# Performance work log

Hardware: AMD Instinct MI355X
Metric: run time of the kernel (lower is better)

The kernel has to match this reference:

```python
import jax, jax.numpy as jnp
import numpy as np

N = 4096
D_IN = 1024
D_OUT = 1024
NUM_HEADS = 16
HEAD_DIM = D_OUT // NUM_HEADS


def setup_inputs() -> dict:
    key = jax.random.key(0)
    ks = jax.random.split(key, 7)
    scale = 1.0 / np.sqrt(D_IN)
    return {
        "q": jax.random.normal(ks[0], (N, D_IN), dtype=jnp.float32),
        "k": jax.random.normal(ks[1], (N, D_IN), dtype=jnp.float32),
        "v": jax.random.normal(ks[2], (N, D_IN), dtype=jnp.float32),
        "W_q": jax.random.normal(ks[3], (D_IN, D_OUT), dtype=jnp.float32) * scale,
        "W_k": jax.random.normal(ks[4], (D_IN, D_OUT), dtype=jnp.float32) * scale,
        "W_v": jax.random.normal(ks[5], (D_IN, D_OUT), dtype=jnp.float32) * scale,
        "W_o": jax.random.normal(ks[6], (D_OUT, D_OUT), dtype=jnp.float32) * scale,
    }


def reference(q, k, v, W_q, W_k, W_v, W_o):
    n = q.shape[0]
    # QKV projections -> [h, n, d]
    Q = (q @ W_q).reshape(n, NUM_HEADS, HEAD_DIM).transpose(1, 0, 2)
    K = (k @ W_k).reshape(n, NUM_HEADS, HEAD_DIM).transpose(1, 0, 2)
    V = (v @ W_v).reshape(n, NUM_HEADS, HEAD_DIM).transpose(1, 0, 2)
    scores = jnp.einsum('hid,hjd->hij', Q, K) / jnp.sqrt(jnp.float32(HEAD_DIM))
    attn = jax.nn.softmax(scores, axis=-1)  # dropout p=0.0 (eval) -> no-op
    h = jnp.einsum('hij,hjd->hid', attn, V)
    h = h.transpose(1, 0, 2).reshape(n, D_OUT)
    return h @ W_o
```

## Files before the change

kernel.cpp:

```cpp
#include <hip/hip_runtime.h>
#include <math.h>

#define NTOK   4096
#define DMODEL 1024
#define NHEADS 16
#define HDIM   64
#define KDIM   1024

typedef __attribute__((ext_vector_type(8))) short          bf16x8;
typedef __attribute__((ext_vector_type(4))) float          f32x4;
typedef __attribute__((ext_vector_type(16))) float         f32x16;
typedef __attribute__((ext_vector_type(4))) unsigned int   u32x4;
typedef __attribute__((ext_vector_type(4))) unsigned short us4;

static __device__ __forceinline__ unsigned short f2bf(float f) {
    unsigned int u = __float_as_uint(f);
    u += 0x7fffu + ((u >> 16) & 1u);
    return (unsigned short)(u >> 16);
}

static __device__ __forceinline__ unsigned int pk2bf(float a, float b) {
#if __has_builtin(__builtin_amdgcn_cvt_pk_bf16_f32)
    return __builtin_bit_cast(unsigned int,
                              __builtin_amdgcn_cvt_pk_bf16_f32(a, b));
#else
    unsigned int ua = __float_as_uint(a) + 0x8000u;
    unsigned int ub = __float_as_uint(b) + 0x8000u;
    return __builtin_amdgcn_perm(ub, ua, 0x07060302u);
#endif
}

#if __has_builtin(__builtin_amdgcn_exp2f)
#define EXP2(x) __builtin_amdgcn_exp2f(x)
#else
#define EXP2(x) exp2f(x)
#endif

static __device__ __forceinline__ void async_copy16(void* lds, const void* g) {
    __builtin_amdgcn_global_load_lds(
        (const __attribute__((address_space(1))) unsigned int*)g,
        (__attribute__((address_space(3))) unsigned int*)lds, 16, 0, 0);
}

static __device__ __forceinline__ unsigned int comb2(unsigned int x,
                                                     unsigned int y,
                                                     float inv) {
    float x0 = __uint_as_float(x << 16);
    float x1 = __uint_as_float(x & 0xffff0000u);
    float y0 = __uint_as_float(y << 16);
    float y1 = __uint_as_float(y & 0xffff0000u);
    return pk2bf((x0 + y0) * inv, (x1 + y1) * inv);
}

__global__ __launch_bounds__(256)
void cast_wt_kernel(const float* __restrict__ Wq, const float* __restrict__ Wk,
                    const float* __restrict__ Wv, const float* __restrict__ Wo,
                    unsigned short* __restrict__ Tq, unsigned short* __restrict__ Tk,
                    unsigned short* __restrict__ Tv, unsigned short* __restrict__ To) {
    __shared__ float Ws[64][65];
    const float* W;
    unsigned short* T;
    switch (blockIdx.z) {
        case 0:  W = Wq; T = Tq; break;
        case 1:  W = Wk; T = Tk; break;
        case 2:  W = Wv; T = Tv; break;
        default: W = Wo; T = To; break;
    }
    const int k0 = blockIdx.x * 64, n0 = blockIdx.y * 64;
    const int t = threadIdx.x;
    #pragma unroll
    for (int i = 0; i < 4; i++) {
        int c  = i * 256 + t;
        int kk = c >> 4;
        int n4 = (c & 15) << 2;
        *(float4*)(&Ws[kk][n4]) =
            *(const float4*)(W + (size_t)(k0 + kk) * DMODEL + n0 + n4);
    }
    __syncthreads();
    #pragma unroll
    for (int i = 0; i < 4; i++) {
        int c  = i * 256 + t;
        int nn = c >> 4;
        int k4 = (c & 15) << 2;
        us4 o = { f2bf(Ws[k4 + 0][nn]), f2bf(Ws[k4 + 1][nn]),
                  f2bf(Ws[k4 + 2][nn]), f2bf(Ws[k4 + 3][nn]) };
        *(us4*)(T + (size_t)(n0 + nn) * KDIM + k0 + k4) = o;
    }
}

__global__ __launch_bounds__(256)
void cast_in_kernel(const float* __restrict__ q, const float* __restrict__ k,
                    const float* __restrict__ v,
                    unsigned short* __restrict__ Qb,
                    unsigned short* __restrict__ Kb,
                    unsigned short* __restrict__ Vb) {
    const float* src;
    unsigned short* dst;
    switch (blockIdx.y) {
        case 0:  src = q; dst = Qb; break;
        case 1:  src = k; dst = Kb; break;
        default: src = v; dst = Vb; break;
    }
    size_t i = ((size_t)blockIdx.x * 256 + threadIdx.x) * 8;
    float4 f0 = *(const float4*)(src + i);
    float4 f1 = *(const float4*)(src + i + 4);
    uint2 o0 = { pk2bf(f0.x, f0.y), pk2bf(f0.z, f0.w) };
    uint2 o1 = { pk2bf(f1.x, f1.y), pk2bf(f1.z, f1.w) };
    *(uint2*)(dst + i)     = o0;
    *(uint2*)(dst + i + 4) = o1;
}

__global__ __launch_bounds__(256, 3)
void qkv_gemm_pre(const unsigned short* __restrict__ Qb,
                  const unsigned short* __restrict__ Kb,
                  const unsigned short* __restrict__ Vb,
                  const unsigned short* __restrict__ Btq,
                  const unsigned short* __restrict__ Btk,
                  const unsigned short* __restrict__ Btv,
                  unsigned short* __restrict__ Oq, unsigned short* __restrict__ Ok,
                  unsigned short* __restrict__ Ov) {
    __shared__ unsigned short As[128 * 64];
    __shared__ unsigned short Bs[128 * 64];

    const unsigned short* A;
    const unsigned short* Bt;
    unsigned short* Out;
    int mode;
    float sc;
    switch (blockIdx.z) {
        case 0:  A = Qb; Bt = Btq; Out = Oq; mode = 1; sc = 0.18033688011112042f; break;
        case 1:  A = Kb; Bt = Btk; Out = Ok; mode = 1; sc = 1.0f; break;
        default: A = Vb; Bt = Btv; Out = Ov; mode = 2; sc = 1.0f; break;
    }

    const int t    = threadIdx.x;
    const int w    = t >> 6;
    const int lane = t & 63;
    const int quad = lane >> 4;
    const int l15  = lane & 15;
    const int wr   = w >> 1, wc = w & 1;
    const int bm   = blockIdx.y * 128, bn = blockIdx.x * 128;

    f32x4 acc[4][4];
    #pragma unroll
    for (int i = 0; i < 4; i++)
        #pragma unroll
        for (int j = 0; j < 4; j++) acc[i][j] = (f32x4)(0.f);

    for (int k0 = 0; k0 < KDIM; k0 += 64) {
        __syncthreads();
        #pragma unroll
        for (int i = 0; i < 4; i++) {
            int cb = (i * 4 + w) * 64;
            int c  = cb + lane;
            int r  = c >> 3;
            int ko = (c & 7) * 8;
            async_copy16((void*)(Bs + cb * 8),
                         (const void*)(Bt + (size_t)(bn + r) * KDIM + k0 + ko));
            async_copy16((void*)(As + cb * 8),
                         (const void*)(A + (size_t)(bm + r) * KDIM + k0 + ko));
        }
        __syncthreads();
        #pragma unroll
        for (int kq = 0; kq < 2; kq++) {
            bf16x8 af[4], bf[4];
            #pragma unroll
            for (int mt = 0; mt < 4; mt++)
                af[mt] = *(bf16x8*)(As + (wr * 64 + mt * 16 + l15) * 64 + kq * 32 + quad * 8);
            #pragma unroll
            for (int nt = 0; nt < 4; nt++)
                bf[nt] = *(bf16x8*)(Bs + (wc * 64 + nt * 16 + l15) * 64 + kq * 32 + quad * 8);
            #pragma unroll
            for (int mt = 0; mt < 4; mt++)
                #pragma unroll
                for (int nt = 0; nt < 4; nt++)
                    acc[mt][nt] = __builtin_amdgcn_mfma_f32_16x16x32_bf16(
                        af[mt], bf[nt], acc[mt][nt], 0, 0, 0);
        }
    }

    #pragma unroll
    for (int mt = 0; mt < 4; mt++) {
        #pragma unroll
        for (int nt = 0; nt < 4; nt++) {
            int col  = bn + wc * 64 + nt * 16 + l15;
            int row0 = bm + wr * 64 + mt * 16 + quad * 4;
            if (mode == 1) {
                size_t base = ((size_t)(col >> 6)) * NTOK * HDIM + (col & 63);
                #pragma unroll
                for (int r = 0; r < 4; r++)
                    Out[base + (size_t)(row0 + r) * HDIM] = f2bf(acc[mt][nt][r] * sc);
            } else {
                size_t base = ((size_t)(col >> 6)) * HDIM * NTOK +
                              (size_t)(col & 63) * NTOK + row0;
                us4 o = { f2bf(acc[mt][nt][0]), f2bf(acc[mt][nt][1]),
                          f2bf(acc[mt][nt][2]), f2bf(acc[mt][nt][3]) };
                *(us4*)(Out + base) = o;
            }
        }
    }
}

__global__ __launch_bounds__(256, 3)
void qkv_gemm(const float* __restrict__ Aq, const float* __restrict__ Ak,
              const float* __restrict__ Av,
              const unsigned short* __restrict__ Btq,
              const unsigned short* __restrict__ Btk,
              const unsigned short* __restrict__ Btv,
              unsigned short* __restrict__ Oq, unsigned short* __restrict__ Ok,
              unsigned short* __restrict__ Ov) {
    __shared__ unsigned short As[128 * 64];
    __shared__ unsigned short Bs[128 * 64];

    const float* A;
    const unsigned short* Bt;
    unsigned short* Out;
    int mode;
    float sc;
    switch (blockIdx.z) {
        case 0:  A = Aq; Bt = Btq; Out = Oq; mode = 1; sc = 0.18033688011112042f; break;
        case 1:  A = Ak; Bt = Btk; Out = Ok; mode = 1; sc = 1.0f; break;
        default: A = Av; Bt = Btv; Out = Ov; mode = 2; sc = 1.0f; break;
    }

    const int t    = threadIdx.x;
    const int w    = t >> 6;
    const int lane = t & 63;
    const int quad = lane >> 4;
    const int l15  = lane & 15;
    const int wr   = w >> 1, wc = w & 1;
    const int bm   = blockIdx.y * 128, bn = blockIdx.x * 128;

    f32x4 acc[4][4];
    #pragma unroll
    for (int i = 0; i < 4; i++)
        #pragma unroll
        for (int j = 0; j < 4; j++) acc[i][j] = (f32x4)(0.f);

    for (int k0 = 0; k0 < KDIM; k0 += 64) {
        __syncthreads();
        #pragma unroll
        for (int i = 0; i < 4; i++) {
            int cb = (i * 4 + w) * 64;
            int c  = cb + lane;
            int r  = c >> 3;
            int ko = (c & 7) * 8;
            async_copy16((void*)(Bs + cb * 8),
                         (const void*)(Bt + (size_t)(bn + r) * KDIM + k0 + ko));
        }
        #pragma unroll
        for (int i = 0; i < 4; i++) {
            int c2 = i * 256 + t;
            int r  = c2 >> 3;
            int k8 = (c2 & 7) * 8;
            const float* src = A + (size_t)(bm + r) * KDIM + k0 + k8;
            float4 f0 = *(const float4*)(src);
            float4 f1 = *(const float4*)(src + 4);
            uint2 p0 = { pk2bf(f0.x, f0.y), pk2bf(f0.z, f0.w) };
            uint2 p1 = { pk2bf(f1.x, f1.y), pk2bf(f1.z, f1.w) };
            *(uint2*)(As + r * 64 + k8)     = p0;
            *(uint2*)(As + r * 64 + k8 + 4) = p1;
        }
        __syncthreads();
        #pragma unroll
        for (int kq = 0; kq < 2; kq++) {
            bf16x8 af[4], bf[4];
            #pragma unroll
            for (int mt = 0; mt < 4; mt++)
                af[mt] = *(bf16x8*)(As + (wr * 64 + mt * 16 + l15) * 64 + kq * 32 + quad * 8);
            #pragma unroll
            for (int nt = 0; nt < 4; nt++)
                bf[nt] = *(bf16x8*)(Bs + (wc * 64 + nt * 16 + l15) * 64 + kq * 32 + quad * 8);
            #pragma unroll
            for (int mt = 0; mt < 4; mt++)
                #pragma unroll
                for (int nt = 0; nt < 4; nt++)
                    acc[mt][nt] = __builtin_amdgcn_mfma_f32_16x16x32_bf16(
                        af[mt], bf[nt], acc[mt][nt], 0, 0, 0);
        }
    }

    #pragma unroll
    for (int mt = 0; mt < 4; mt++) {
        #pragma unroll
        for (int nt = 0; nt < 4; nt++) {
            int col  = bn + wc * 64 + nt * 16 + l15;
            int row0 = bm + wr * 64 + mt * 16 + quad * 4;
            if (mode == 1) {
                size_t base = ((size_t)(col >> 6)) * NTOK * HDIM + (col & 63);
                #pragma unroll
                for (int r = 0; r < 4; r++)
                    Out[base + (size_t)(row0 + r) * HDIM] = f2bf(acc[mt][nt][r] * sc);
            } else {
                size_t base = ((size_t)(col >> 6)) * HDIM * NTOK +
                              (size_t)(col & 63) * NTOK + row0;
                us4 o = { f2bf(acc[mt][nt][0]), f2bf(acc[mt][nt][1]),
                          f2bf(acc[mt][nt][2]), f2bf(acc[mt][nt][3]) };
                *(us4*)(Out + base) = o;
            }
        }
    }
}

__global__ __launch_bounds__(256, 3)
void out_gemm(const unsigned short* __restrict__ A,
              const unsigned short* __restrict__ Bt,
              float* __restrict__ Out) {
    __shared__ unsigned short As[64 * 64];
    __shared__ unsigned short Bs[128 * 64];

    const int t    = threadIdx.x;
    const int w    = t >> 6;
    const int lane = t & 63;
    const int quad = lane >> 4;
    const int l15  = lane & 15;
    const int wr   = w >> 1, wc = w & 1;
    const int bm   = blockIdx.y * 64, bn = blockIdx.x * 128;

    f32x4 acc[2][4];
    #pragma unroll
    for (int i = 0; i < 2; i++)
        #pragma unroll
        for (int j = 0; j < 4; j++) acc[i][j] = (f32x4)(0.f);

    for (int k0 = 0; k0 < KDIM; k0 += 64) {
        __syncthreads();
        #pragma unroll
        for (int i = 0; i < 4; i++) {
            int cb = (i * 4 + w) * 64;
            int c  = cb + lane;
            int r  = c >> 3;
            int ko = (c & 7) * 8;
            async_copy16((void*)(Bs + cb * 8),
                         (const void*)(Bt + (size_t)(bn + r) * KDIM + k0 + ko));
        }
        #pragma unroll
        for (int i = 0; i < 2; i++) {
            int cb = (i * 4 + w) * 64;
            int c  = cb + lane;
            int r  = c >> 3;
            int ko = (c & 7) * 8;
            async_copy16((void*)(As + cb * 8),
                         (const void*)(A + (size_t)(bm + r) * KDIM + k0 + ko));
        }
        __syncthreads();
        #pragma unroll
        for (int kq = 0; kq < 2; kq++) {
            bf16x8 af[2], bf[4];
            #pragma unroll
            for (int mt = 0; mt < 2; mt++)
                af[mt] = *(bf16x8*)(As + (wr * 32 + mt * 16 + l15) * 64 + kq * 32 + quad * 8);
            #pragma unroll
            for (int nt = 0; nt < 4; nt++)
                bf[nt] = *(bf16x8*)(Bs + (wc * 64 + nt * 16 + l15) * 64 + kq * 32 + quad * 8);
            #pragma unroll
            for (int mt = 0; mt < 2; mt++)
                #pragma unroll
                for (int nt = 0; nt < 4; nt++)
                    acc[mt][nt] = __builtin_amdgcn_mfma_f32_16x16x32_bf16(
                        af[mt], bf[nt], acc[mt][nt], 0, 0, 0);
        }
    }

    #pragma unroll
    for (int mt = 0; mt < 2; mt++) {
        #pragma unroll
        for (int nt = 0; nt < 4; nt++) {
            int col  = bn + wc * 64 + nt * 16 + l15;
            int row0 = bm + wr * 32 + mt * 16 + quad * 4;
            #pragma unroll
            for (int r = 0; r < 4; r++)
                Out[(size_t)(row0 + r) * DMODEL + col] = acc[mt][nt][r];
        }
    }
}

__global__ __launch_bounds__(256, 3)
void out_gemm_comb(const unsigned short* __restrict__ POa,
                   const float* __restrict__ lbuf,
                   const unsigned short* __restrict__ Bt,
                   float* __restrict__ Out) {
    __shared__ unsigned short As[64 * 64];
    __shared__ unsigned short Bs[128 * 64];

    const unsigned short* POb = POa + (size_t)NTOK * DMODEL;

    const int t    = threadIdx.x;
    const int w    = t >> 6;
    const int lane = t & 63;
    const int quad = lane >> 4;
    const int l15  = lane & 15;
    const int wr   = w >> 1, wc = w & 1;
    const int bm   = blockIdx.y * 64, bn = blockIdx.x * 128;

    f32x4 acc[2][4];
    #pragma unroll
    for (int i = 0; i < 2; i++)
        #pragma unroll
        for (int j = 0; j < 4; j++) acc[i][j] = (f32x4)(0.f);

    for (int k0 = 0; k0 < KDIM; k0 += 64) {
        __syncthreads();
        #pragma unroll
        for (int i = 0; i < 4; i++) {
            int cb = (i * 4 + w) * 64;
            int c  = cb + lane;
            int r  = c >> 3;
            int ko = (c & 7) * 8;
            async_copy16((void*)(Bs + cb * 8),
                         (const void*)(Bt + (size_t)(bn + r) * KDIM + k0 + ko));
        }
        #pragma unroll
        for (int i = 0; i < 2; i++) {
            int c   = i * 256 + t;
            int r   = c >> 3;
            int k8  = (c & 7) * 8;
            size_t row = (size_t)(bm + r);
            int col = k0 + k8;
            int hh  = col >> 6;
            uint4 a = *(const uint4*)(POa + row * DMODEL + col);
            uint4 b = *(const uint4*)(POb + row * DMODEL + col);
            float la = lbuf[(size_t)hh * NTOK + row];
            float lb = lbuf[(size_t)NHEADS * NTOK + (size_t)hh * NTOK + row];
            float inv = 1.f / (la + lb);
            uint4 o = { comb2(a.x, b.x, inv), comb2(a.y, b.y, inv),
                        comb2(a.z, b.z, inv), comb2(a.w, b.w, inv) };
            *(uint4*)(As + r * 64 + k8) = o;
        }
        __syncthreads();
        #pragma unroll
        for (int kq = 0; kq < 2; kq++) {
            bf16x8 af[2], bf[4];
            #pragma unroll
            for (int mt = 0; mt < 2; mt++)
                af[mt] = *(bf16x8*)(As + (wr * 32 + mt * 16 + l15) * 64 + kq * 32 + quad * 8);
            #pragma unroll
            for (int nt = 0; nt < 4; nt++)
                bf[nt] = *(bf16x8*)(Bs + (wc * 64 + nt * 16 + l15) * 64 + kq * 32 + quad * 8);
            #pragma unroll
            for (int mt = 0; mt < 2; mt++)
                #pragma unroll
                for (int nt = 0; nt < 4; nt++)
                    acc[mt][nt] = __builtin_amdgcn_mfma_f32_16x16x32_bf16(
                        af[mt], bf[nt], acc[mt][nt], 0, 0, 0);
        }
    }

    #pragma unroll
    for (int mt = 0; mt < 2; mt++) {
        #pragma unroll
        for (int nt = 0; nt < 4; nt++) {
            int col  = bn + wc * 64 + nt * 16 + l15;
            int row0 = bm + wr * 32 + mt * 16 + quad * 4;
            #pragma unroll
            for (int r = 0; r < 4; r++)
                Out[(size_t)(row0 + r) * DMODEL + col] = acc[mt][nt][r];
        }
    }
}

__global__ __launch_bounds__(256, 4)
void attn_split(const unsigned short* __restrict__ Q,
                const unsigned short* __restrict__ K,
                const unsigned short* __restrict__ Vt,
                unsigned short* __restrict__ PO,
                float* __restrict__ lbuf) {
    __shared__ __align__(16) unsigned short Ks[2 * 4096];
    __shared__ __align__(16) unsigned short Vs[2 * 4096];

    const int qt   = blockIdx.x;
    const int h    = blockIdx.y;
    const int half = blockIdx.z;
    const int t    = threadIdx.x;
    const int w    = t >> 6;
    const int lane = t & 63;
    const int r    = lane & 31;
    const int hi   = lane >> 5;
    const int xh   = (r & 7) ^ hi;

    const unsigned short* Qg =
        Q + ((size_t)h * NTOK + qt * 128 + w * 32 + r) * HDIM + hi * 8;
    bf16x8 qf[4];
    #pragma unroll
    for (int ds = 0; ds < 4; ds++)
        qf[ds] = *(const bf16x8*)(Qg + ds * 16);

    const unsigned short* Kg = K  + ((size_t)h * NTOK + half * 2048) * HDIM;
    const unsigned short* Vg = Vt + (size_t)h * HDIM * NTOK + half * 2048;

    const int rr = t >> 3;
    const int oo = ((t & 7) ^ (rr & 7)) * 8;
    const unsigned short* kbase = Kg + (size_t)rr * HDIM + oo;
    const unsigned short* vbase = Vg + (size_t)rr * NTOK + oo;
    unsigned short* ksd = Ks + w * 512;
    unsigned short* vsd = Vs + w * 512;

    auto stage = [&](int kt, int b) {
        const unsigned short* kp = kbase + (size_t)kt * 64 * HDIM;
        const unsigned short* vp = vbase + kt * 64;
        async_copy16((void*)(ksd + b * 4096),        (const void*)kp);
        async_copy16((void*)(ksd + b * 4096 + 2048), (const void*)(kp + 32 * HDIM));
        async_copy16((void*)(vsd + b * 4096),        (const void*)vp);
        async_copy16((void*)(vsd + b * 4096 + 2048), (const void*)(vp + (size_t)32 * NTOK));
    };

    f32x16 O0 = (f32x16)(0.f), O1 = (f32x16)(0.f);
    float l0 = 0.f, l1 = 0.f, l2 = 0.f, l3 = 0.f;

    stage(0, 0);

    for (int kt = 0; kt < 32; kt++) {
        const int cur = kt & 1;
        __syncthreads();
        if (kt + 1 < 32) stage(kt + 1, cur ^ 1);

        const unsigned short* Kb = Ks + cur * 4096 + r * 64;
        const unsigned short* Vb = Vs + cur * 4096 + r * 64;

        f32x16 S0 = (f32x16)(0.f), S1 = (f32x16)(0.f);
        #pragma unroll
        for (int ds = 0; ds < 4; ds++) {
            int c = ((2 * ds) ^ xh) * 8;
            bf16x8 k0 = *(const bf16x8*)(Kb + c);
            bf16x8 k1 = *(const bf16x8*)(Kb + 2048 + c);
            S0 = __builtin_amdgcn_mfma_f32_32x32x16_bf16(k0, qf[ds], S0, 0, 0, 0);
            S1 = __builtin_amdgcn_mfma_f32_32x32x16_bf16(k1, qf[ds], S1, 0, 0, 0);
        }

        #pragma unroll
        for (int kb = 0; kb < 2; kb++) {
            const f32x16 S = kb ? S1 : S0;
            float p[16];
            #pragma unroll
            for (int i = 0; i < 16; i++) p[i] = EXP2(S[i]);
            #pragma unroll
            for (int i = 0; i < 4; i++) {
                l0 += p[i * 4 + 0];
                l1 += p[i * 4 + 1];
                l2 += p[i * 4 + 2];
                l3 += p[i * 4 + 3];
            }
            #pragma unroll
            for (int g = 0; g < 2; g++) {
                unsigned int w0 = pk2bf(p[g * 8 + 0], p[g * 8 + 1]);
                unsigned int w2 = pk2bf(p[g * 8 + 4], p[g * 8 + 5]);
                unsigned int w1 = pk2bf(p[g * 8 + 2], p[g * 8 + 3]);
                unsigned int w3 = pk2bf(p[g * 8 + 6], p[g * 8 + 7]);
                asm volatile("v_permlane32_swap_b32 %0, %1" : "+v"(w0), "+v"(w2));
                asm volatile("v_permlane32_swap_b32 %0, %1" : "+v"(w1), "+v"(w3));
                u32x4 pw = { w0, w1, w2, w3 };
                bf16x8 pf = __builtin_bit_cast(bf16x8, pw);
                int kg = kb * 2 + g;
                int c  = ((2 * kg) ^ xh) * 8;
                bf16x8 v0 = *(const bf16x8*)(Vb + c);
                bf16x8 v1 = *(const bf16x8*)(Vb + 2048 + c);
                O0 = __builtin_amdgcn_mfma_f32_32x32x16_bf16(v0, pf, O0, 0, 0, 0);
                O1 = __builtin_amdgcn_mfma_f32_32x32x16_bf16(v1, pf, O1, 0, 0, 0);
            }
        }
    }

    float lt  = (l0 + l1) + (l2 + l3);
    float ltot = lt + __shfl_xor(lt, 32, 64);

    unsigned short* POh = PO + (size_t)half * NTOK * DMODEL;
    size_t row = (size_t)qt * 128 + w * 32 + r;
    unsigned short* dst = POh + row * DMODEL + h * HDIM;
    #pragma unroll
    for (int db = 0; db < 2; db++) {
        const f32x16 O = db ? O1 : O0;
        #pragma unroll
        for (int g = 0; g < 4; g++) {
            int d = db * 32 + g * 8 + hi * 4;
            uint2 o = { pk2bf(O[g * 4 + 0], O[g * 4 + 1]),
                        pk2bf(O[g * 4 + 2], O[g * 4 + 3]) };
            *(uint2*)(dst + d) = o;
        }
    }
    if (hi == 0)
        lbuf[((size_t)half * NHEADS + h) * NTOK + row] = ltot;
}

__global__ __launch_bounds__(256)
void attn_mfma(const unsigned short* __restrict__ Q,
               const unsigned short* __restrict__ K,
               const unsigned short* __restrict__ Vt,
               unsigned short* __restrict__ ctx) {
    __shared__ __align__(16) unsigned short Ks[2 * 4096];
    __shared__ __align__(16) unsigned short Vs[2 * 4096];
    __shared__ __align__(16) unsigned short Ps[4][32][72];

    const int h    = blockIdx.y;
    const int qt   = blockIdx.x;
    const int t    = threadIdx.x;
    const int w    = t >> 6;
    const int lane = t & 63;
    const int quad = lane >> 4;
    const int l15  = lane & 15;

    const unsigned short* Qg =
        Q + ((size_t)h * NTOK + qt * 128 + w * 32 + l15) * HDIM;
    bf16x8 qf[2][2];
    qf[0][0] = *(const bf16x8*)(Qg + quad * 8);
    qf[0][1] = *(const bf16x8*)(Qg + 32 + quad * 8);
    qf[1][0] = *(const bf16x8*)(Qg + 16 * HDIM + quad * 8);
    qf[1][1] = *(const bf16x8*)(Qg + 16 * HDIM + 32 + quad * 8);

    const unsigned short* Kg = K  + (size_t)h * NTOK * HDIM;
    const unsigned short* Vg = Vt + (size_t)h * HDIM * NTOK;

    const int rr = t >> 3;
    const int oo = ((t & 7) ^ (rr & 7)) * 8;
    const unsigned short* kbase = Kg + (size_t)rr * HDIM + oo;
    const unsigned short* vbase = Vg + (size_t)rr * NTOK + oo;
    unsigned short* ksd = Ks + w * 512;
    unsigned short* vsd = Vs + w * 512;

    auto stage = [&](int kt, int b) {
        const unsigned short* kp = kbase + (size_t)kt * 64 * HDIM;
        const unsigned short* vp = vbase + kt * 64;
        async_copy16((void*)(ksd + b * 4096),        (const void*)kp);
        async_copy16((void*)(ksd + b * 4096 + 2048), (const void*)(kp + 32 * HDIM));
        async_copy16((void*)(vsd + b * 4096),        (const void*)vp);
        async_copy16((void*)(vsd + b * 4096 + 2048), (const void*)(vp + (size_t)32 * NTOK));
    };

    const int xb = l15 & 7;
    const int a0 = l15 * 64 + ((quad    ) ^ xb) * 8;
    const int a1 = l15 * 64 + ((quad + 4) ^ xb) * 8;

    const bf16x8 ones = { 16256, 16256, 16256, 16256,
                          16256, 16256, 16256, 16256 };

    f32x4 O[2][4];
    f32x4 lacc[2];
    #pragma unroll
    for (int tl = 0; tl < 2; tl++) {
        lacc[tl] = (f32x4)(0.f);
        #pragma unroll
        for (int dt = 0; dt < 4; dt++) O[tl][dt] = (f32x4)(0.f);
    }

    stage(0, 0);

    for (int kt = 0; kt < NTOK / 64; kt++) {
        const int cur = kt & 1;
        __syncthreads();
        if (kt + 1 < NTOK / 64) stage(kt + 1, cur ^ 1);

        f32x4 s[2][4];
        #pragma unroll
        for (int kc = 0; kc < 4; kc++) {
            bf16x8 kf0 = *(bf16x8*)(Ks + cur * 4096 + kc * 1024 + a0);
            bf16x8 kf1 = *(bf16x8*)(Ks + cur * 4096 + kc * 1024 + a1);
            #pragma unroll
            for (int tl = 0; tl < 2; tl++) {
                f32x4 acc = (f32x4)(0.f);
                acc = __builtin_amdgcn_mfma_f32_16x16x32_bf16(kf0, qf[tl][0], acc, 0, 0, 0);
                acc = __builtin_amdgcn_mfma_f32_16x16x32_bf16(kf1, qf[tl][1], acc, 0, 0, 0);
                s[tl][kc] = acc;
            }
        }

        bf16x8 vf[4][2];
        #pragma unroll
        for (int dt = 0; dt < 4; dt++) {
            vf[dt][0] = *(bf16x8*)(Vs + cur * 4096 + dt * 1024 + a0);
            vf[dt][1] = *(bf16x8*)(Vs + cur * 4096 + dt * 1024 + a1);
        }

        #pragma unroll
        for (int tl = 0; tl < 2; tl++) {
            #pragma unroll
            for (int kc = 0; kc < 4; kc++) {
                float e0 = EXP2(s[tl][kc][0]);
                float e1 = EXP2(s[tl][kc][1]);
                float e2 = EXP2(s[tl][kc][2]);
                float e3 = EXP2(s[tl][kc][3]);
                uint2 p = { pk2bf(e0, e1), pk2bf(e2, e3) };
                *(uint2*)(&Ps[w][tl * 16 + l15][kc * 16 + quad * 4]) = p;
            }
            asm volatile("s_waitcnt lgkmcnt(0)" ::: "memory");

            bf16x8 pf0 = *(bf16x8*)(&Ps[w][tl * 16 + l15][quad * 8]);
            bf16x8 pf1 = *(bf16x8*)(&Ps[w][tl * 16 + l15][32 + quad * 8]);
            lacc[tl] = __builtin_amdgcn_mfma_f32_16x16x32_bf16(ones, pf0, lacc[tl], 0, 0, 0);
            lacc[tl] = __builtin_amdgcn_mfma_f32_16x16x32_bf16(ones, pf1, lacc[tl], 0, 0, 0);
            #pragma unroll
            for (int dt = 0; dt < 4; dt++) {
                O[tl][dt] = __builtin_amdgcn_mfma_f32_16x16x32_bf16(vf[dt][0], pf0, O[tl][dt], 0, 0, 0);
                O[tl][dt] = __builtin_amdgcn_mfma_f32_16x16x32_bf16(vf[dt][1], pf1, O[tl][dt], 0, 0, 0);
            }
        }
    }

    #pragma unroll
    for (int tl = 0; tl < 2; tl++) {
        float inv = 1.f / lacc[tl][0];
        size_t row = (size_t)qt * 128 + w * 32 + tl * 16 + l15;
        #pragma unroll
        for (int dt = 0; dt < 4; dt++) {
            uint2 o = { pk2bf(O[tl][dt][0] * inv, O[tl][dt][1] * inv),
                        pk2bf(O[tl][dt][2] * inv, O[tl][dt][3] * inv) };
            *(uint2*)(ctx + row * DMODEL + h * HDIM + dt * 16 + quad * 4) = o;
        }
    }
}

extern "C" void kernel_launch(void* const* d_in, const int* in_sizes, int n_in,
                              void* d_out, int out_size, void* d_ws, size_t ws_size,
                              hipStream_t stream) {
    const float* q  = (const float*)d_in[0];
    const float* k  = (const float*)d_in[1];
    const float* v  = (const float*)d_in[2];
    const float* Wq = (const float*)d_in[3];
    const float* Wk = (const float*)d_in[4];
    const float* Wv = (const float*)d_in[5];
    const float* Wo = (const float*)d_in[6];
    float* out = (float*)d_out;

    unsigned short* WqT = (unsigned short*)d_ws;
    unsigned short* WkT = WqT + (size_t)DMODEL * KDIM;
    unsigned short* WvT = WkT + (size_t)DMODEL * KDIM;
    unsigned short* WoT = WvT + (size_t)DMODEL * KDIM;
    unsigned short* Qh  = WoT + (size_t)DMODEL * KDIM;
    unsigned short* Kh  = Qh  + (size_t)NTOK * DMODEL;
    unsigned short* Vth = Kh  + (size_t)NTOK * DMODEL;
    unsigned short* ctx = Vth + (size_t)NTOK * DMODEL;
    unsigned short* Qb  = ctx + (size_t)NTOK * DMODEL;
    unsigned short* Kb  = Qb  + (size_t)NTOK * DMODEL;
    unsigned short* Vb  = Kb  + (size_t)NTOK * DMODEL;
    unsigned short* PO  = Qb;
    float*          lb  = (float*)(PO + (size_t)2 * NTOK * DMODEL);

    const bool bigws = ws_size >= (size_t)67108864;

    cast_wt_kernel<<<dim3(16, 16, 4), 256, 0, stream>>>(Wq, Wk, Wv, Wo,
                                                        WqT, WkT, WvT, WoT);
    if (bigws) {
        cast_in_kernel<<<dim3(2048, 3), 256, 0, stream>>>(q, k, v, Qb, Kb, Vb);
        qkv_gemm_pre<<<dim3(DMODEL / 128, NTOK / 128, 3), 256, 0, stream>>>(
            Qb, Kb, Vb, WqT, WkT, WvT, Qh, Kh, Vth);
        attn_split<<<dim3(NTOK / 128, NHEADS, 2), 256, 0, stream>>>(
            Qh, Kh, Vth, PO, lb);
        out_gemm_comb<<<dim3(DMODEL / 128, NTOK / 64), 256, 0, stream>>>(
            PO, lb, WoT, out);
    } else {
        qkv_gemm<<<dim3(DMODEL / 128, NTOK / 128, 3), 256, 0, stream>>>(
            q, k, v, WqT, WkT, WvT, Qh, Kh, Vth);
        attn_mfma<<<dim3(NTOK / 128, NHEADS), 256, 0, stream>>>(Qh, Kh, Vth, ctx);
        out_gemm<<<dim3(DMODEL / 128, NTOK / 64), 256, 0, stream>>>(ctx, WoT, out);
    }
}
```

Baseline: 257.8 us.

## Halve attn_split block and KV tile to 64 queries and 32 keys

The split-KV attention kernel now runs 128-thread blocks covering 64 query rows, and streams 32-key K/V tiles over 64 iterations instead of 64-key tiles over 32. The staging swizzle and shared-memory layout are reworked for the narrower V tile. The grid doubles, so more blocks are resident per CU and each uses less LDS, which should help occupancy and latency hiding. In exchange, each loaded K/V tile is shared by fewer query rows, so global/L2 traffic per query rises, and there are twice as many barriers per block.

```diff
diff --git a/kernel.cpp b/kernel.cpp
--- a/kernel.cpp
+++ b/kernel.cpp
@@ -459,14 +459,14 @@
     }
 }
 
-__global__ __launch_bounds__(256, 4)
+__global__ __launch_bounds__(128, 4)
 void attn_split(const unsigned short* __restrict__ Q,
                 const unsigned short* __restrict__ K,
                 const unsigned short* __restrict__ Vt,
                 unsigned short* __restrict__ PO,
                 float* __restrict__ lbuf) {
-    __shared__ __align__(16) unsigned short Ks[2 * 4096];
-    __shared__ __align__(16) unsigned short Vs[2 * 4096];
+    __shared__ __align__(16) unsigned short Ks[2 * 2048];
+    __shared__ __align__(16) unsigned short Vs[2 * 2048];
 
     const int qt   = blockIdx.x;
     const int h    = blockIdx.y;
@@ -476,10 +476,11 @@
     const int lane = t & 63;
     const int r    = lane & 31;
     const int hi   = lane >> 5;
-    const int xh   = (r & 7) ^ hi;
+    const int xh8  = (r & 7) ^ hi;
+    const int xh4  = (r & 3) ^ hi;
 
     const unsigned short* Qg =
-        Q + ((size_t)h * NTOK + qt * 128 + w * 32 + r) * HDIM + hi * 8;
+        Q + ((size_t)h * NTOK + qt * 64 + w * 32 + r) * HDIM + hi * 8;
     bf16x8 qf[4];
     #pragma unroll
     for (int ds = 0; ds < 4; ds++)
@@ -488,20 +489,23 @@
     const unsigned short* Kg = K  + ((size_t)h * NTOK + half * 2048) * HDIM;
     const unsigned short* Vg = Vt + (size_t)h * HDIM * NTOK + half * 2048;
 
-    const int rr = t >> 3;
-    const int oo = ((t & 7) ^ (rr & 7)) * 8;
-    const unsigned short* kbase = Kg + (size_t)rr * HDIM + oo;
-    const unsigned short* vbase = Vg + (size_t)rr * NTOK + oo;
+    const int krow = t >> 3;
+    const int koo  = ((t & 7) ^ (krow & 7)) * 8;
+    const unsigned short* kbase = Kg + (size_t)krow * HDIM + koo;
+    const int vrow = t >> 2;
+    const int voo  = ((t & 3) ^ (vrow & 3)) * 8;
+    const unsigned short* vbase = Vg + (size_t)vrow * NTOK + voo;
+
     unsigned short* ksd = Ks + w * 512;
     unsigned short* vsd = Vs + w * 512;
 
     auto stage = [&](int kt, int b) {
-        const unsigned short* kp = kbase + (size_t)kt * 64 * HDIM;
-        const unsigned short* vp = vbase + kt * 64;
-        async_copy16((void*)(ksd + b * 4096),        (const void*)kp);
-        async_copy16((void*)(ksd + b * 4096 + 2048), (const void*)(kp + 32 * HDIM));
-        async_copy16((void*)(vsd + b * 4096),        (const void*)vp);
-        async_copy16((void*)(vsd + b * 4096 + 2048), (const void*)(vp + (size_t)32 * NTOK));
+        const unsigned short* kp = kbase + (size_t)kt * 32 * HDIM;
+        const unsigned short* vp = vbase + kt * 32;
+        async_copy16((void*)(ksd + b * 2048),        (const void*)kp);
+        async_copy16((void*)(ksd + b * 2048 + 1024), (const void*)(kp + 16 * HDIM));
+        async_copy16((void*)(vsd + b * 2048),        (const void*)vp);
+        async_copy16((void*)(vsd + b * 2048 + 1024), (const void*)(vp + (size_t)32 * NTOK));
     };
 
     f32x16 O0 = (f32x16)(0.f), O1 = (f32x16)(0.f);
@@ -509,62 +513,54 @@
 
     stage(0, 0);
 
-    for (int kt = 0; kt < 32; kt++) {
+    for (int kt = 0; kt < 64; kt++) {
         const int cur = kt & 1;
         __syncthreads();
-        if (kt + 1 < 32) stage(kt + 1, cur ^ 1);
-
-        const unsigned short* Kb = Ks + cur * 4096 + r * 64;
-        const unsigned short* Vb = Vs + cur * 4096 + r * 64;
-
-        f32x16 S0 = (f32x16)(0.f), S1 = (f32x16)(0.f);
+        if (kt + 1 < 64) stage(kt + 1, cur ^ 1);
+
+        const unsigned short* Kb = Ks + cur * 2048 + r * 64;
+        const unsigned short* Vb = Vs + cur * 2048 + r * 32;
+
+        f32x16 S = (f32x16)(0.f);
         #pragma unroll
         for (int ds = 0; ds < 4; ds++) {
-            int c = ((2 * ds) ^ xh) * 8;
-            bf16x8 k0 = *(const bf16x8*)(Kb + c);
-            bf16x8 k1 = *(const bf16x8*)(Kb + 2048 + c);
-            S0 = __builtin_amdgcn_mfma_f32_32x32x16_bf16(k0, qf[ds], S0, 0, 0, 0);
-            S1 = __builtin_amdgcn_mfma_f32_32x32x16_bf16(k1, qf[ds], S1, 0, 0, 0);
-        }
-
-        #pragma unroll
-        for (int kb = 0; kb < 2; kb++) {
-            const f32x16 S = kb ? S1 : S0;
-            float p[16];
-            #pragma unroll
-            for (int i = 0; i < 16; i++) p[i] = EXP2(S[i]);
-            #pragma unroll
-            for (int i = 0; i < 4; i++) {
-                l0 += p[i * 4 + 0];
-                l1 += p[i * 4 + 1];
-                l2 += p[i * 4 + 2];
-                l3 += p[i * 4 + 3];
-            }
-            #pragma unroll
-            for (int g = 0; g < 2; g++) {
-                unsigned int w0 = pk2bf(p[g * 8 + 0], p[g * 8 + 1]);
-                unsigned int w2 = pk2bf(p[g * 8 + 4], p[g * 8 + 5]);
-                unsigned int w1 = pk2bf(p[g * 8 + 2], p[g * 8 + 3]);
-                unsigned int w3 = pk2bf(p[g * 8 + 6], p[g * 8 + 7]);
-                asm volatile("v_permlane32_swap_b32 %0, %1" : "+v"(w0), "+v"(w2));
-                asm volatile("v_permlane32_swap_b32 %0, %1" : "+v"(w1), "+v"(w3));
-                u32x4 pw = { w0, w1, w2, w3 };
-                bf16x8 pf = __builtin_bit_cast(bf16x8, pw);
-                int kg = kb * 2 + g;
-                int c  = ((2 * kg) ^ xh) * 8;
-                bf16x8 v0 = *(const bf16x8*)(Vb + c);
-                bf16x8 v1 = *(const bf16x8*)(Vb + 2048 + c);
-                O0 = __builtin_amdgcn_mfma_f32_32x32x16_bf16(v0, pf, O0, 0, 0, 0);
-                O1 = __builtin_amdgcn_mfma_f32_32x32x16_bf16(v1, pf, O1, 0, 0, 0);
-            }
-        }
-    }
-
-    float lt  = (l0 + l1) + (l2 + l3);
+            bf16x8 kf = *(const bf16x8*)(Kb + ((2 * ds) ^ xh8) * 8);
+            S = __builtin_amdgcn_mfma_f32_32x32x16_bf16(kf, qf[ds], S, 0, 0, 0);
+        }
+
+        #pragma unroll
+        for (int kg = 0; kg < 2; kg++) {
+            float p0 = EXP2(S[kg * 8 + 0]);
+            float p1 = EXP2(S[kg * 8 + 1]);
+            float p2 = EXP2(S[kg * 8 + 2]);
+            float p3 = EXP2(S[kg * 8 + 3]);
+            float p4 = EXP2(S[kg * 8 + 4]);
+            float p5 = EXP2(S[kg * 8 + 5]);
+            float p6 = EXP2(S[kg * 8 + 6]);
+            float p7 = EXP2(S[kg * 8 + 7]);
+            l0 += p0; l1 += p1; l2 += p2; l3 += p3;
+            l0 += p4; l1 += p5; l2 += p6; l3 += p7;
+            unsigned int w0 = pk2bf(p0, p1);
+            unsigned int w2 = pk2bf(p4, p5);
+            unsigned int w1 = pk2bf(p2, p3);
+            unsigned int w3 = pk2bf(p6, p7);
+            asm volatile("v_permlane32_swap_b32 %0, %1" : "+v"(w0), "+v"(w2));
+            asm volatile("v_permlane32_swap_b32 %0, %1" : "+v"(w1), "+v"(w3));
+            u32x4 pw = { w0, w1, w2, w3 };
+            bf16x8 pf = __builtin_bit_cast(bf16x8, pw);
+            int cv = ((2 * kg) ^ xh4) * 8;
+            bf16x8 v0 = *(const bf16x8*)(Vb + cv);
+            bf16x8 v1 = *(const bf16x8*)(Vb + 1024 + cv);
+            O0 = __builtin_amdgcn_mfma_f32_32x32x16_bf16(v0, pf, O0, 0, 0, 0);
+            O1 = __builtin_amdgcn_mfma_f32_32x32x16_bf16(v1, pf, O1, 0, 0, 0);
+        }
+    }
+
+    float lt   = (l0 + l1) + (l2 + l3);
     float ltot = lt + __shfl_xor(lt, 32, 64);
 
     unsigned short* POh = PO + (size_t)half * NTOK * DMODEL;
-    size_t row = (size_t)qt * 128 + w * 32 + r;
+    size_t row = (size_t)qt * 64 + w * 32 + r;
     unsigned short* dst = POh + row * DMODEL + h * HDIM;
     #pragma unroll
     for (int db = 0; db < 2; db++) {
@@ -741,7 +737,7 @@
         cast_in_kernel<<<dim3(2048, 3), 256, 0, stream>>>(q, k, v, Qb, Kb, Vb);
         qkv_gemm_pre<<<dim3(DMODEL / 128, NTOK / 128, 3), 256, 0, stream>>>(
             Qb, Kb, Vb, WqT, WkT, WvT, Qh, Kh, Vth);
-        attn_split<<<dim3(NTOK / 128, NHEADS, 2), 256, 0, stream>>>(
+        attn_split<<<dim3(NTOK / 64, NHEADS, 2), 128, 0, stream>>>(
             Qh, Kh, Vth, PO, lb);
         out_gemm_comb<<<dim3(DMODEL / 128, NTOK / 64), 256, 0, stream>>>(
             PO, lb, WoT, out);
```

After: 281.1 us. 1.09x slower.
